# Performance work log

Measured on AMD Instinct MI355X. Metric: run time of the kernel, lower is better.

Reference implementation:

```python
import jax, jax.numpy as jnp
import numpy as np

NB, MS, T, IN, H, OUT, DOCS, ENT = 512, 8, 64, 360, 230, 53, 32, 8


def setup_inputs() -> dict:
    key = jax.random.key(0)
    ks = jax.random.split(key, 16)
    s = 0.05
    inp = {
        "bag": jax.random.normal(ks[0], (NB, MS, T, IN), jnp.float32),
        "W_ih_f": jax.random.normal(ks[1], (3 * H, IN), jnp.float32) * s,
        "W_hh_f": jax.random.normal(ks[2], (3 * H, H), jnp.float32) * s,
        "b_ih_f": jnp.zeros((3 * H,), jnp.float32),
        "b_hh_f": jnp.zeros((3 * H,), jnp.float32),
        "W_ih_r": jax.random.normal(ks[3], (3 * H, IN), jnp.float32) * s,
        "W_hh_r": jax.random.normal(ks[4], (3 * H, H), jnp.float32) * s,
        "b_ih_r": jnp.zeros((3 * H,), jnp.float32),
        "b_hh_r": jnp.zeros((3 * H,), jnp.float32),
        "W_word": jax.random.normal(ks[5], (2 * H, 2 * H), jnp.float32) * s,
        "b_word": jnp.zeros((2 * H,), jnp.float32),
        "proj_word": jax.random.normal(ks[6], (2 * H,), jnp.float32) * s,
        "W_sent": jax.random.normal(ks[7], (2 * H, 2 * H), jnp.float32) * s,
        "b_sent": jnp.zeros((2 * H,), jnp.float32),
        "proj_sent": jax.random.normal(ks[8], (2 * H,), jnp.float32) * s,
        "fc_W": jax.random.normal(ks[9], (OUT, 2 * H), jnp.float32) * s,
        "fc_b": jnp.zeros((OUT,), jnp.float32),
    }
    # unique (doc, ent_a, ent_b) triples with a != b, as the Python bag loop produces
    rng = np.random.RandomState(0)
    grid = np.stack(np.meshgrid(np.arange(DOCS), np.arange(ENT), np.arange(ENT), indexing="ij"), -1).reshape(-1, 3)
    grid = grid[grid[:, 1] != grid[:, 2]]
    inp["pairs"] = jnp.asarray(grid[rng.permutation(len(grid))[:NB]], jnp.int32)
    return inp


def _gru_dir(xg, W_hh, b_hh, reverse):
    # xg: [T, B, 3H] precomputed input-gate projections; torch gate order r,z,n
    def step(h, xt):
        hg = h @ W_hh.T + b_hh  # [B, 3H]
        r = jax.nn.sigmoid(xt[:, :H] + hg[:, :H])
        z = jax.nn.sigmoid(xt[:, H:2 * H] + hg[:, H:2 * H])
        n = jnp.tanh(xt[:, 2 * H:] + r * hg[:, 2 * H:])
        h2 = (1.0 - z) * n + z * h
        return h2, h2
    h0 = jnp.zeros((xg.shape[1], H), xg.dtype)
    _, hs = jax.lax.scan(step, h0, xg, reverse=reverse)
    return hs  # [T, B, H], time-aligned


def reference(bag, W_ih_f, W_hh_f, b_ih_f, b_hh_f, W_ih_r, W_hh_r, b_ih_r, b_hh_r,
              W_word, b_word, proj_word, W_sent, b_sent, proj_sent, fc_W, fc_b, pairs):
    B = NB * MS
    # every sentence of every bag runs through the same GRU -> batch them all
    x = bag.reshape(B, T, IN).transpose(1, 0, 2)  # [T, B, IN]
    hf = _gru_dir(x @ W_ih_f.T + b_ih_f, W_hh_f, b_hh_f, reverse=False)
    hr = _gru_dir(x @ W_ih_r.T + b_ih_r, W_hh_r, b_hh_r, reverse=True)
    out = jnp.concatenate([hf, hr], axis=-1)  # [T, B, 2H]
    # word-level tanh attention over time
    u = jnp.tanh(out @ W_word + b_word)
    alpha = jax.nn.softmax(u @ proj_word, axis=0)  # [T, B]
    word_vec = jnp.einsum("tb,tbh->bh", alpha, out)  # [B, 2H]
    word_vec = word_vec.reshape(NB, MS, 2 * H).transpose(1, 0, 2)  # [MS, NB, 2H]
    # sentence-level tanh attention over sentences in each bag
    u2 = jnp.tanh(word_vec @ W_sent + b_sent)
    beta = jax.nn.softmax(u2 @ proj_sent, axis=0)  # [MS, NB]
    sent_vec = jnp.einsum("sb,sbh->bh", beta, word_vec)  # [NB, 2H]
    bag_out = sent_vec @ fc_W.T + fc_b  # [NB, OUT]
    # scatter bag outputs into the dense (doc, ent_a, ent_b) result tensor
    bags_res = jnp.zeros((DOCS, ENT, ENT, OUT), bag_out.dtype)
    bags_res = bags_res.at[pairs[:, 0], pairs[:, 1], pairs[:, 2]].set(bag_out)
    return bags_res
```

## Files before the change

kernel.cpp:

```cpp
#include <hip/hip_runtime.h>
#include <math.h>

typedef __bf16 bf16;
typedef __bf16 bf16x8 __attribute__((ext_vector_type(8)));
typedef float f32x4 __attribute__((ext_vector_type(4)));
typedef float f4 __attribute__((ext_vector_type(4)));

constexpr int kNB = 512, kMS = 8, kT = 64, kH = 230, kIN = 360, kOUT = 53;
constexpr int kB  = kNB * kMS;
constexpr long kBT = (long)kB * kT;
constexpr int kNP  = 768;
constexpr int kKIH = 384;
constexpr int kKHH = 256;
constexpr int k2H  = 460;
constexpr int kLD  = 464;
constexpr int kKW  = 480;
constexpr int kXS  = 772;
constexpr int kHB  = 268;

__device__ inline float fast_sigmoid(float x) {
    return __builtin_amdgcn_rcpf(1.f + __builtin_amdgcn_exp2f(x * -1.442695040888963f));
}
__device__ inline float fast_tanh(float x) {
    return 1.f - 2.f * __builtin_amdgcn_rcpf(1.f + __builtin_amdgcn_exp2f(x * 2.885390081777927f));
}

__device__ inline void async16(const bf16* g, void* l) {
    __builtin_amdgcn_global_load_lds((const __attribute__((address_space(1))) void*)g,
                                     (__attribute__((address_space(3))) void*)l, 16, 0, 0);
}

constexpr long SZ_XG    = 2L * kB * kT * kNP * 2;
constexpr long SZ_OUT   = kBT * kLD * 2;
constexpr long SZ_WIHP  = 2L * kNP * kKIH * 2;
constexpr long SZ_WHHP  = 2L * kNP * kKHH * 2;
constexpr long SZ_WWT   = 512L * kKW * 2;
constexpr long SZ_WST   = 512L * kKW * 2;
constexpr long SZ_BIHP  = 2L * kNP * 4;
constexpr long SZ_BHHP  = 2L * kNP * 4;
constexpr long SZ_VEC   = 2048L * 4;
constexpr long SZ_SCORE = kBT * 4;
constexpr long SZ_WVF   = (long)kB * kLD * 4;
constexpr long SZ_WVB   = (long)kB * kLD * 2;
constexpr long SZ_S2    = (long)kB * 4;

static inline long align256(long x) { return (x + 255) & ~255L; }

__launch_bounds__(256)
__global__ void convert_bag(const float* __restrict__ bag, bf16* __restrict__ bagb)
{
    const long g = (long)blockIdx.x * 256 + threadIdx.x;
    if (g >= kBT * 48) return;
    const long row = g / 48; const int cb = (int)(g % 48);
    bf16x8 v;
    if (cb < 45) {
        const f4* p = (const f4*)(bag + row * kIN + cb * 8);
        f4 a = p[0], b = p[1];
        v[0]=(bf16)a[0]; v[1]=(bf16)a[1]; v[2]=(bf16)a[2]; v[3]=(bf16)a[3];
        v[4]=(bf16)b[0]; v[5]=(bf16)b[1]; v[6]=(bf16)b[2]; v[7]=(bf16)b[3];
    } else {
        v = bf16x8{};
    }
    *(bf16x8*)(bagb + row * kKIH + cb * 8) = v;
}

constexpr int R0 = 2 * kNP * kKIH;
constexpr int R1 = 2 * kNP * kKHH;
constexpr int R2 = 512 * kKW;
constexpr int R3 = 512 * kKW;
constexpr int R4 = 2 * kNP;
constexpr int R5 = 2 * kNP;
constexpr int R6 = 4 * 512;
constexpr long PREP_TOTAL = (long)R0 + R1 + R2 + R3 + R4 + R5 + R6;

__device__ inline bool unpack_n(int n, int& src) {
    int cb = n / 48, w = n % 48, g = w / 16, cc = w & 15;
    int c = cb * 16 + cc;
    src = g * kH + c;
    return c < kH;
}

__launch_bounds__(256)
__global__ void prep_pack(const float* __restrict__ Wihf, const float* __restrict__ Wihr,
                          const float* __restrict__ Whhf, const float* __restrict__ Whhr,
                          const float* __restrict__ bihf, const float* __restrict__ bihr,
                          const float* __restrict__ bhhf, const float* __restrict__ bhhr,
                          const float* __restrict__ Ww,  const float* __restrict__ bw,
                          const float* __restrict__ pw,
                          const float* __restrict__ Wsn, const float* __restrict__ bs,
                          const float* __restrict__ ps,
                          bf16* __restrict__ WihP, bf16* __restrict__ WhhP,
                          bf16* __restrict__ WwT,  bf16* __restrict__ WsT,
                          float* __restrict__ bihP, float* __restrict__ bhhP,
                          float* __restrict__ vecP)
{
    for (long id = (long)blockIdx.x * 256 + threadIdx.x; id < PREP_TOTAL;
         id += (long)gridDim.x * 256) {
        long i = id;
        if (i < R0) {
            int d = (int)(i / (kNP * kKIH)); int r = (int)(i % (kNP * kKIH));
            int n = r / kKIH, k = r % kKIH;
            int src; bool v = unpack_n(n, src) && (k < kIN);
            WihP[i] = v ? (bf16)(d ? Wihr : Wihf)[(long)src * kIN + k] : (bf16)0.f;
            continue;
        }
        i -= R0;
        if (i < R1) {
            int d = (int)(i / (kNP * kKHH)); int r = (int)(i % (kNP * kKHH));
            int n = r / kKHH, k = r % kKHH;
            int src; bool v = unpack_n(n, src) && (k < kH);
            WhhP[i] = v ? (bf16)(d ? Whhr : Whhf)[(long)src * kH + k] : (bf16)0.f;
            continue;
        }
        i -= R1;
        if (i < R2) {
            int n = (int)(i / kKW), k = (int)(i % kKW);
            WwT[i] = (n < k2H && k < k2H) ? (bf16)Ww[(long)k * k2H + n] : (bf16)0.f;
            continue;
        }
        i -= R2;
        if (i < R3) {
            int n = (int)(i / kKW), k = (int)(i % kKW);
            WsT[i] = (n < k2H && k < k2H) ? (bf16)Wsn[(long)k * k2H + n] : (bf16)0.f;
            continue;
        }
        i -= R3;
        if (i < R4) {
            int d = (int)(i / kNP), n = (int)(i % kNP);
            int src; bool v = unpack_n(n, src);
            bihP[i] = v ? (d ? bihr : bihf)[src] : 0.f;
            continue;
        }
        i -= R4;
        if (i < R5) {
            int d = (int)(i / kNP), n = (int)(i % kNP);
            int src; bool v = unpack_n(n, src);
            bhhP[i] = v ? (d ? bhhr : bhhf)[src] : 0.f;
            continue;
        }
        i -= R5;
        {
            int which = (int)(i / 512), n = (int)(i % 512);
            const float* s = (which == 0) ? bw : (which == 1) ? pw : (which == 2) ? bs : ps;
            vecP[i] = (n < k2H) ? s[n] : 0.f;
        }
    }
}

template<int MODE>
__launch_bounds__(256)
__global__ void gemm_k(const bf16* __restrict__ A, int lda, int ksteps,
                       const bf16* __restrict__ Bp, long bStride,
                       bf16* __restrict__ C, int ldc, long cStride,
                       const float* __restrict__ bias, int biasStride,
                       const float* __restrict__ proj,
                       float* __restrict__ score,
                       int nblks, int zc)
{
    __shared__ bf16 As[128][32];
    __shared__ bf16 Bs[128][32];
    const int tid = threadIdx.x;
    const int grp = 8 * nblks * zc;
    const int mg = blockIdx.x / grp, sub = blockIdx.x % grp;
    const int mi = sub & 7, rest = sub >> 3;
    const int nblk = rest % nblks, z = rest / nblks;
    const int mblk = mg * 8 + mi;

    const bf16* Bz = Bp + (long)z * bStride;
    const int rowA0 = mblk * 128, rowB0 = nblk * 128;
    const int lane = tid & 63, wave = tid >> 6;
    const int wm = wave >> 1, wn = wave & 1;
    const int quad = lane >> 4, l16 = lane & 15;
    const int ldb = ksteps * 32;

    const int sr = lane >> 2, scb = (lane & 3) * 8;
    const bf16* gA0 = A + (long)(rowA0 + wave * 16 + sr) * lda + scb;
    const bf16* gA1 = gA0 + (long)64 * lda;
    const bf16* gB0 = Bz + (long)(rowB0 + wave * 16 + sr) * ldb + scb;
    const bf16* gB1 = gB0 + (long)64 * ldb;
    void* lA0 = &As[wave * 16][0];
    void* lA1 = &As[64 + wave * 16][0];
    void* lB0 = &Bs[wave * 16][0];
    void* lB1 = &Bs[64 + wave * 16][0];

    f32x4 acc[4][4] = {};

    for (int ks = 0; ks < ksteps; ++ks) {
        const int kk = ks * 32;
        async16(gA0 + kk, lA0);
        async16(gA1 + kk, lA1);
        async16(gB0 + kk, lB0);
        async16(gB1 + kk, lB1);
        __syncthreads();
        bf16x8 af[4], bfr[4];
#pragma unroll
        for (int mt = 0; mt < 4; ++mt) af[mt] = *(const bf16x8*)&As[wm * 64 + mt * 16 + l16][quad * 8];
#pragma unroll
        for (int nt = 0; nt < 4; ++nt) bfr[nt] = *(const bf16x8*)&Bs[wn * 64 + nt * 16 + l16][quad * 8];
#pragma unroll
        for (int mt = 0; mt < 4; ++mt)
#pragma unroll
            for (int nt = 0; nt < 4; ++nt)
                acc[mt][nt] = __builtin_amdgcn_mfma_f32_16x16x32_bf16(af[mt], bfr[nt], acc[mt][nt], 0, 0, 0);
        __syncthreads();
    }

    if constexpr (MODE == 0 || MODE == 2) {
        bf16* Cz = C + (long)z * cStride;
        const float* bz = bias + (long)z * biasStride;
#pragma unroll
        for (int mt = 0; mt < 4; ++mt)
#pragma unroll
            for (int nt = 0; nt < 4; ++nt) {
                const int col = rowB0 + wn * 64 + nt * 16 + l16;
                const float bv = bz[col];
#pragma unroll
                for (int r = 0; r < 4; ++r) {
                    const int row = rowA0 + wm * 64 + mt * 16 + quad * 4 + r;
                    const int rowp = (MODE == 2) ? ((row & 63) * kB + (row >> 6)) : row;
                    Cz[(long)rowp * ldc + col] = (bf16)(acc[mt][nt][r] + bv);
                }
            }
    } else {
#pragma unroll
        for (int mt = 0; mt < 4; ++mt)
#pragma unroll
            for (int r = 0; r < 4; ++r) {
                float s = 0.f;
#pragma unroll
                for (int nt = 0; nt < 4; ++nt) {
                    const int col = rowB0 + wn * 64 + nt * 16 + l16;
                    s += fast_tanh(acc[mt][nt][r] + bias[col]) * proj[col];
                }
                for (int m = 1; m < 16; m <<= 1) s += __shfl_xor(s, m, 64);
                if (l16 == 0) {
                    const int row = rowA0 + wm * 64 + mt * 16 + quad * 4 + r;
                    atomicAdd(&score[row], s);
                }
            }
    }
}

__launch_bounds__(512)
__global__ void gru_rec(const bf16* __restrict__ xg,
                        const bf16* __restrict__ Whh,
                        const float* __restrict__ bhh,
                        bf16* __restrict__ outbuf)
{
    __shared__ bf16 hbf[32][kHB];
    __shared__ bf16 xs[32][kXS];
    const int tid = threadIdx.x;
    const int d = blockIdx.y;
    const int row0 = blockIdx.x * 32;
    const int lane = tid & 63, wave = tid >> 6;
    const int quad = lane >> 4, l16 = lane & 15;
    const int cb0 = wave * 2;

    for (int i = tid; i < 32 * kHB; i += 512) (&hbf[0][0])[i] = (bf16)0.f;

    const bf16* xgd = xg + (long)d * ((long)kT * kB * kNP);
    const bf16* Wd  = Whh + (long)d * ((long)kNP * kKHH);
    const float* bd = bhh + (long)d * kNP;

    float hreg[2][2][4] = {};
    float bdr[2], bdz[2], bdn[2];
#pragma unroll
    for (int cbl = 0; cbl < 2; ++cbl) {
        const int cb = cb0 + cbl;
        bdr[cbl] = bd[cb * 48 + l16];
        bdz[cbl] = bd[cb * 48 + 16 + l16];
        bdn[cbl] = bd[cb * 48 + 32 + l16];
    }

    const int xr_row = tid >> 4, xr_col = (tid & 15) * 48;

    bf16x8 pf[6];
    {
        const int t0 = d ? kT - 1 : 0;
        const bf16* src = xgd + ((long)t0 * kB + row0) * kNP + (long)tid * 48;
#pragma unroll
        for (int j = 0; j < 6; ++j) pf[j] = *(const bf16x8*)(src + j * 8);
    }
    __syncthreads();

    for (int it = 0; it < kT; ++it) {
        const int t = d ? (kT - 1 - it) : it;
#pragma unroll
        for (int j = 0; j < 6; ++j) *(bf16x8*)&xs[xr_row][xr_col + j * 8] = pf[j];

        f32x4 acc[2][2][3] = {};
#pragma unroll
        for (int ks = 0; ks < 8; ++ks) {
            bf16x8 af0 = *(const bf16x8*)&hbf[l16][ks * 32 + quad * 8];
            bf16x8 af1 = *(const bf16x8*)&hbf[16 + l16][ks * 32 + quad * 8];
#pragma unroll
            for (int cbl = 0; cbl < 2; ++cbl)
#pragma unroll
                for (int g = 0; g < 3; ++g) {
                    const int n = (cb0 + cbl) * 48 + g * 16 + l16;
                    bf16x8 bfr = *(const bf16x8*)(Wd + (long)n * kKHH + ks * 32 + quad * 8);
                    acc[0][cbl][g] = __builtin_amdgcn_mfma_f32_16x16x32_bf16(af0, bfr, acc[0][cbl][g], 0, 0, 0);
                    acc[1][cbl][g] = __builtin_amdgcn_mfma_f32_16x16x32_bf16(af1, bfr, acc[1][cbl][g], 0, 0, 0);
                }
        }
        if (it + 1 < kT) {
            const int tn = d ? (kT - 2 - it) : (it + 1);
            const bf16* src = xgd + ((long)tn * kB + row0) * kNP + (long)tid * 48;
#pragma unroll
            for (int j = 0; j < 6; ++j) pf[j] = *(const bf16x8*)(src + j * 8);
        }
        __syncthreads();

#pragma unroll
        for (int cbl = 0; cbl < 2; ++cbl) {
            const int cb = cb0 + cbl;
            const int c = cb * 16 + l16;
            if (c < kH) {
#pragma unroll
                for (int mt = 0; mt < 2; ++mt)
#pragma unroll
                    for (int r = 0; r < 4; ++r) {
                        const int rl = mt * 16 + quad * 4 + r;
                        const float xr = (float)xs[rl][cb * 48 + l16];
                        const float xz = (float)xs[rl][cb * 48 + 16 + l16];
                        const float xn = (float)xs[rl][cb * 48 + 32 + l16];
                        const float rgate = fast_sigmoid(xr + acc[mt][cbl][0][r] + bdr[cbl]);
                        const float zgate = fast_sigmoid(xz + acc[mt][cbl][1][r] + bdz[cbl]);
                        const float ngate = fast_tanh(xn + rgate * (acc[mt][cbl][2][r] + bdn[cbl]));
                        const float h2 = (1.f - zgate) * ngate + zgate * hreg[mt][cbl][r];
                        hreg[mt][cbl][r] = h2;
                        hbf[rl][c] = (bf16)h2;
                        outbuf[((long)(row0 + rl) * kT + t) * kLD + d * kH + c] = (bf16)h2;
                    }
            }
        }
        __syncthreads();
    }
}

__launch_bounds__(256)
__global__ void word_attn(const float* __restrict__ score, const bf16* __restrict__ outbuf,
                          float* __restrict__ wvf, bf16* __restrict__ wvb)
{
    const int b = blockIdx.x, tid = threadIdx.x;
    __shared__ float alpha[kT];
    if (tid < 64) {
        float v = score[b * kT + tid];
        float m = v;
        for (int off = 32; off; off >>= 1) m = fmaxf(m, __shfl_xor(m, off, 64));
        float e = __builtin_amdgcn_exp2f((v - m) * 1.442695040888963f);
        float s = e;
        for (int off = 32; off; off >>= 1) s += __shfl_xor(s, off, 64);
        alpha[tid] = e / s;
    }
    __syncthreads();
    const bf16* base = outbuf + (long)b * kT * kLD;
    float a0 = 0.f, a1 = 0.f;
    const int c0 = tid, c1 = tid + 256;
#pragma unroll 4
    for (int t = 0; t < kT; ++t) {
        const float al = alpha[t];
        a0 += al * (float)base[t * kLD + c0];
        if (c1 < k2H) a1 += al * (float)base[t * kLD + c1];
    }
    wvf[(long)b * kLD + c0] = a0;
    wvb[(long)b * kLD + c0] = (bf16)a0;
    if (c1 < k2H) {
        wvf[(long)b * kLD + c1] = a1;
        wvb[(long)b * kLD + c1] = (bf16)a1;
    }
}

__launch_bounds__(256)
__global__ void final_sent(const float* __restrict__ score2, const float* __restrict__ wvf,
                           const float* __restrict__ fcW, const float* __restrict__ fcb,
                           const int* __restrict__ pairs, float* __restrict__ outp)
{
    const int nb = blockIdx.x, tid = threadIdx.x;
    __shared__ float beta[kMS];
    __shared__ float sv[k2H];
    if (tid == 0) {
        float m = -1e30f;
        for (int s = 0; s < kMS; ++s) m = fmaxf(m, score2[nb * kMS + s]);
        float e[kMS], sum = 0.f;
        for (int s = 0; s < kMS; ++s) { e[s] = expf(score2[nb * kMS + s] - m); sum += e[s]; }
        for (int s = 0; s < kMS; ++s) beta[s] = e[s] / sum;
    }
    __syncthreads();
    for (int c = tid; c < k2H; c += 256) {
        float a = 0.f;
#pragma unroll
        for (int s = 0; s < kMS; ++s) a += beta[s] * wvf[(long)(nb * kMS + s) * kLD + c];
        sv[c] = a;
    }
    __syncthreads();
    const int lane = tid & 63, wave = tid >> 6;
    const long base = ((long)pairs[nb * 3] * 64 + pairs[nb * 3 + 1] * 8 + pairs[nb * 3 + 2]) * kOUT;
    for (int o = wave; o < kOUT; o += 4) {
        float p = 0.f;
        for (int c = lane; c < k2H; c += 64) p += sv[c] * fcW[(long)o * k2H + c];
        for (int off = 32; off; off >>= 1) p += __shfl_xor(p, off, 64);
        if (lane == 0) outp[base + o] = p + fcb[o];
    }
}

extern "C" void kernel_launch(void* const* d_in, const int* in_sizes, int n_in,
                              void* d_out, int out_size, void* d_ws, size_t ws_size,
                              hipStream_t stream)
{
    const float* bag  = (const float*)d_in[0];
    const float* Wihf = (const float*)d_in[1];
    const float* Whhf = (const float*)d_in[2];
    const float* bihf = (const float*)d_in[3];
    const float* bhhf = (const float*)d_in[4];
    const float* Wihr = (const float*)d_in[5];
    const float* Whhr = (const float*)d_in[6];
    const float* bihr = (const float*)d_in[7];
    const float* bhhr = (const float*)d_in[8];
    const float* Ww   = (const float*)d_in[9];
    const float* bw   = (const float*)d_in[10];
    const float* pw   = (const float*)d_in[11];
    const float* Wsn  = (const float*)d_in[12];
    const float* bs   = (const float*)d_in[13];
    const float* ps   = (const float*)d_in[14];
    const float* fcW  = (const float*)d_in[15];
    const float* fcb  = (const float*)d_in[16];
    const int* pairs  = (const int*)d_in[17];

    char* ws = (char*)d_ws;
    long off = 0;
    auto alloc = [&](long sz) { void* p = ws + off; off += align256(sz); return p; };
    bf16* xg    = (bf16*)alloc(SZ_XG);
    bf16* outb  = (bf16*)alloc(SZ_OUT);
    bf16* bagb  = outb;
    bf16* WihP  = (bf16*)alloc(SZ_WIHP);
    bf16* WhhP  = (bf16*)alloc(SZ_WHHP);
    bf16* WwT   = (bf16*)alloc(SZ_WWT);
    bf16* WsT   = (bf16*)alloc(SZ_WST);
    float* bihP = (float*)alloc(SZ_BIHP);
    float* bhhP = (float*)alloc(SZ_BHHP);
    float* vecP = (float*)alloc(SZ_VEC);
    float* score= (float*)alloc(SZ_SCORE);
    float* wvf  = (float*)alloc(SZ_WVF);
    bf16* wvb   = (bf16*)alloc(SZ_WVB);
    float* s2   = (float*)alloc(SZ_S2);
    if ((size_t)off > ws_size) return;

    hipMemsetAsync(d_out, 0, (size_t)out_size * 4, stream);
    hipMemsetAsync(score, 0, SZ_SCORE, stream);
    hipMemsetAsync(s2, 0, SZ_S2, stream);

    convert_bag<<<(int)((kBT * 48 + 255) / 256), 256, 0, stream>>>(bag, bagb);

    prep_pack<<<5781, 256, 0, stream>>>(Wihf, Wihr, Whhf, Whhr, bihf, bihr, bhhf, bhhr,
                                        Ww, bw, pw, Wsn, bs, ps,
                                        WihP, WhhP, WwT, WsT, bihP, bhhP, vecP);

    gemm_k<2><<<2048 * 6 * 2, 256, 0, stream>>>(bagb, kKIH, 12,
                                                WihP, (long)kNP * kKIH,
                                                xg, kNP, (long)kT * kB * kNP,
                                                bihP, kNP, nullptr, nullptr, 6, 2);

    gru_rec<<<dim3(128, 2), 512, 0, stream>>>(xg, WhhP, bhhP, outb);

    gemm_k<1><<<2048 * 4, 256, 0, stream>>>(outb, kLD, 15,
                                            WwT, 0, nullptr, 0, 0,
                                            vecP, 0, vecP + 512, score, 4, 1);

    word_attn<<<kB, 256, 0, stream>>>(score, outb, wvf, wvb);

    gemm_k<1><<<32 * 4, 256, 0, stream>>>(wvb, kLD, 15,
                                          WsT, 0, nullptr, 0, 0,
                                          vecP + 1024, 0, vecP + 1536, s2, 4, 1);

    final_sent<<<kNB, 256, 0, stream>>>(s2, wvf, fcW, fcb, pairs, (float*)d_out);
}
```

Baseline: 2.154 ms.

## Cache recurrent weight fragments in registers and stream gate inputs asynchronously into LDS

The GRU recurrence kernel now loads the W_hh B-fragments for the first 6 of 8 k-steps once into registers before the time loop. This avoids re-reading them from global memory/cache on every timestep. The per-step input-gate prefetch, which went through registers and then an LDS store, is replaced with direct global-to-LDS async loads issued after the step's final barrier into an unpadded xs buffer. Occupancy is also requested at 2 blocks per CU. The cost is much higher register pressure, with possible spills or a lower real occupancy. The unpadded LDS row stride may also cause bank conflicts when gate inputs are read.

Measured after the change: 2.296 ms. 1.07x slower.

```diff
diff --git a/kernel.cpp b/kernel.cpp
--- a/kernel.cpp
+++ b/kernel.cpp
@@ -15,7 +15,6 @@
 constexpr int k2H  = 460;
 constexpr int kLD  = 464;
 constexpr int kKW  = 480;
-constexpr int kXS  = 772;
 constexpr int kHB  = 268;
 
 __device__ inline float fast_sigmoid(float x) {
@@ -241,14 +240,14 @@
     }
 }
 
-__launch_bounds__(512)
+__launch_bounds__(512, 2)
 __global__ void gru_rec(const bf16* __restrict__ xg,
                         const bf16* __restrict__ Whh,
                         const float* __restrict__ bhh,
                         bf16* __restrict__ outbuf)
 {
     __shared__ bf16 hbf[32][kHB];
-    __shared__ bf16 xs[32][kXS];
+    __shared__ bf16 xs[32 * kNP];
     const int tid = threadIdx.x;
     const int d = blockIdx.y;
     const int row0 = blockIdx.x * 32;
@@ -272,21 +271,28 @@
         bdn[cbl] = bd[cb * 48 + 32 + l16];
     }
 
-    const int xr_row = tid >> 4, xr_col = (tid & 15) * 48;
-
-    bf16x8 pf[6];
+    bf16x8 wc[6][2][3];
+#pragma unroll
+    for (int ks = 0; ks < 6; ++ks)
+#pragma unroll
+        for (int cbl = 0; cbl < 2; ++cbl)
+#pragma unroll
+            for (int g = 0; g < 3; ++g) {
+                const int n = (cb0 + cbl) * 48 + g * 16 + l16;
+                wc[ks][cbl][g] = *(const bf16x8*)(Wd + (long)n * kKHH + ks * 32 + quad * 8);
+            }
+
     {
         const int t0 = d ? kT - 1 : 0;
-        const bf16* src = xgd + ((long)t0 * kB + row0) * kNP + (long)tid * 48;
-#pragma unroll
-        for (int j = 0; j < 6; ++j) pf[j] = *(const bf16x8*)(src + j * 8);
+        const bf16* src = xgd + ((long)t0 * kB + row0) * kNP + wave * 3072 + lane * 8;
+#pragma unroll
+        for (int j = 0; j < 6; ++j)
+            async16(src + j * 512, &xs[wave * 3072 + j * 512]);
     }
     __syncthreads();
 
     for (int it = 0; it < kT; ++it) {
         const int t = d ? (kT - 1 - it) : it;
-#pragma unroll
-        for (int j = 0; j < 6; ++j) *(bf16x8*)&xs[xr_row][xr_col + j * 8] = pf[j];
 
         f32x4 acc[2][2][3] = {};
 #pragma unroll
@@ -297,17 +303,16 @@
             for (int cbl = 0; cbl < 2; ++cbl)
 #pragma unroll
                 for (int g = 0; g < 3; ++g) {
-                    const int n = (cb0 + cbl) * 48 + g * 16 + l16;
-                    bf16x8 bfr = *(const bf16x8*)(Wd + (long)n * kKHH + ks * 32 + quad * 8);
-                    acc[0][cbl][g] = __builtin_amdgcn_mfma_f32_16x16x32_bf16(af0, bfr, acc[0][cbl][g], 0, 0, 0);
-                    acc[1][cbl][g] = __builtin_amdgcn_mfma_f32_16x16x32_bf16(af1, bfr, acc[1][cbl][g], 0, 0, 0);
+                    bf16x8 b;
+                    if (ks < 6) {
+                        b = wc[ks][cbl][g];
+                    } else {
+                        const int n = (cb0 + cbl) * 48 + g * 16 + l16;
+                        b = *(const bf16x8*)(Wd + (long)n * kKHH + ks * 32 + quad * 8);
+                    }
+                    acc[0][cbl][g] = __builtin_amdgcn_mfma_f32_16x16x32_bf16(af0, b, acc[0][cbl][g], 0, 0, 0);
+                    acc[1][cbl][g] = __builtin_amdgcn_mfma_f32_16x16x32_bf16(af1, b, acc[1][cbl][g], 0, 0, 0);
                 }
-        }
-        if (it + 1 < kT) {
-            const int tn = d ? (kT - 2 - it) : (it + 1);
-            const bf16* src = xgd + ((long)tn * kB + row0) * kNP + (long)tid * 48;
-#pragma unroll
-            for (int j = 0; j < 6; ++j) pf[j] = *(const bf16x8*)(src + j * 8);
         }
         __syncthreads();
 
@@ -321,9 +326,10 @@
 #pragma unroll
                     for (int r = 0; r < 4; ++r) {
                         const int rl = mt * 16 + quad * 4 + r;
-                        const float xr = (float)xs[rl][cb * 48 + l16];
-                        const float xz = (float)xs[rl][cb * 48 + 16 + l16];
-                        const float xn = (float)xs[rl][cb * 48 + 32 + l16];
+                        const bf16* xrow = &xs[rl * kNP + cb * 48 + l16];
+                        const float xr = (float)xrow[0];
+                        const float xz = (float)xrow[16];
+                        const float xn = (float)xrow[32];
                         const float rgate = fast_sigmoid(xr + acc[mt][cbl][0][r] + bdr[cbl]);
                         const float zgate = fast_sigmoid(xz + acc[mt][cbl][1][r] + bdz[cbl]);
                         const float ngate = fast_tanh(xn + rgate * (acc[mt][cbl][2][r] + bdn[cbl]));
@@ -335,6 +341,14 @@
             }
         }
         __syncthreads();
+
+        if (it + 1 < kT) {
+            const int tn = d ? (kT - 2 - it) : (it + 1);
+            const bf16* src = xgd + ((long)tn * kB + row0) * kNP + wave * 3072 + lane * 8;
+#pragma unroll
+            for (int j = 0; j < 6; ++j)
+                async16(src + j * 512, &xs[wave * 3072 + j * 512]);
+        }
     }
 }
 
```
